# Performance work log

Hardware: AMD Instinct MI355X
Metric: run time of the kernel (lower is better)

The kernel has to match this reference:

```python
import jax, jax.numpy as jnp
import numpy as np

B, D, H = 131072, 256, 256
E, K, R = 4, 2, 5


def setup_inputs() -> dict:
    key = jax.random.key(0)
    ks = jax.random.split(key, 10)
    z = jax.random.normal(ks[0], (B, D), dtype=jnp.float32)
    centroids = jax.random.normal(ks[1], (R, E, D), dtype=jnp.float32) * 0.5
    tau_raw = jnp.full((R,), np.log(np.e - 1.0), dtype=jnp.float32)  # softplus(tau_raw)=1.0
    # Expert FFN params (Linear init ~ U(-1/sqrt(fan_in), 1/sqrt(fan_in)))
    s1 = 1.0 / np.sqrt(D)
    s2 = 1.0 / np.sqrt(H)
    W1 = jax.random.uniform(ks[2], (E, D, H), dtype=jnp.float32, minval=-s1, maxval=s1)
    b1 = jax.random.uniform(ks[3], (E, H), dtype=jnp.float32, minval=-s1, maxval=s1)
    W2 = jax.random.uniform(ks[4], (E, H, D), dtype=jnp.float32, minval=-s2, maxval=s2)
    b2 = jax.random.uniform(ks[5], (E, D), dtype=jnp.float32, minval=-s2, maxval=s2)
    ln_gamma = jnp.ones((D,), dtype=jnp.float32)
    ln_beta = jnp.zeros((D,), dtype=jnp.float32)
    return {"z": z, "router_idx": 2, "centroids": centroids, "tau_raw": tau_raw,
            "W1": W1, "b1": b1, "W2": W2, "b2": b2,
            "ln_gamma": ln_gamma, "ln_beta": ln_beta}


def reference(z, router_idx, centroids, tau_raw, W1, b1, W2, b2, ln_gamma, ln_beta):
    num_experts = W1.shape[0]
    top_k = K
    c = centroids[router_idx]                       # (E, D)
    tau = jax.nn.softplus(tau_raw[router_idx]) + 1e-6
    # Laplace-kernel gating: exp(-||z - c||_2 / tau)
    dist = jnp.sqrt(jnp.sum((z[:, None, :] - c[None, :, :]) ** 2, axis=-1))  # (B, E)
    scores = jnp.exp(-dist / tau)
    top_scores, top_idx = jax.lax.top_k(scores, top_k)          # (B, K)
    weights = jax.nn.softmax(top_scores, axis=-1)               # (B, K)
    # Dense all-expert FFN (E is tiny), then gather the top-k outputs.
    h = jax.nn.gelu(jnp.einsum('bd,edh->beh', z, W1) + b1[None], approximate=False)
    expert_out = jnp.einsum('beh,ehd->bed', h, W2) + b2[None]   # (B, E, D)
    sel = jnp.take_along_axis(expert_out, top_idx[:, :, None], axis=1)  # (B, K, D)
    moe_out = jnp.sum(weights[:, :, None] * sel, axis=1)        # (B, D)
    # Residual + LayerNorm (eps = 1e-5 as in torch)
    x = z + moe_out
    mu = jnp.mean(x, axis=-1, keepdims=True)
    var = jnp.mean((x - mu) ** 2, axis=-1, keepdims=True)
    y = ln_gamma * (x - mu) / jnp.sqrt(var + 1e-5) + ln_beta
    # Expert utilization (training-mode output)
    counts = jnp.sum(jax.nn.one_hot(top_idx, num_experts, dtype=jnp.float32), axis=(0, 1))
    expert_weights = counts / (z.shape[0] * top_k)
    return y, expert_weights
```

## Files before the change

### kernel.cpp

```cpp
#include <hip/hip_runtime.h>
#include <hip/hip_bf16.h>
#include <math.h>

#define Bz 131072
#define Dd 256

typedef __attribute__((ext_vector_type(8))) short short8;
typedef __attribute__((ext_vector_type(4))) float f32x4;
typedef __attribute__((ext_vector_type(4))) unsigned short u16x4;
typedef __attribute__((ext_vector_type(8))) unsigned short u16x8;

__device__ __forceinline__ unsigned short f2bf(float f) {
    union { __hip_bfloat16 h; unsigned short u; } v;
    v.h = __float2bfloat16(f);
    return v.u;
}
__device__ __forceinline__ float bf2f(unsigned short h) {
    union { unsigned int u; float f; } v; v.u = ((unsigned int)h) << 16;
    return v.f;
}
__device__ __forceinline__ float gelu_f(float x) {
    float u = 0.7978845608028654f * x * (1.0f + 0.044715f * x * x);
    float ex = __builtin_amdgcn_exp2f(u * 2.8853900817779268f);
    float th = 1.0f - 2.0f * __builtin_amdgcn_rcpf(1.0f + ex);
    return 0.5f * x * (1.0f + th);
}

#define MFMA16(a, b, c) __builtin_amdgcn_mfma_f32_16x16x32_bf16(a, b, c, 0, 0, 0)

__global__ __launch_bounds__(256) void prep_kernel(const float* __restrict__ W1,
                                                   const float* __restrict__ W2,
                                                   unsigned short* __restrict__ W1s,
                                                   unsigned short* __restrict__ W2s,
                                                   unsigned int* __restrict__ ctr) {
    __shared__ float tile[32][257];
    int bid = blockIdx.x;
    int tid = threadIdx.x;
    if (bid == 0 && tid < 16) ctr[tid] = 0u;
    int mat = bid >> 5, e = (bid >> 3) & 3, tn = bid & 7;
    const float* src = (mat ? W2 : W1) + e * 65536;
    unsigned short* dst = (mat ? W2s : W1s) + e * 65536 + tn * 8192;
#pragma unroll 4
    for (int kk = 0; kk < 32; ++kk)
        tile[kk][tid] = src[(tn * 32 + kk) * 256 + tid];
    __syncthreads();
#pragma unroll 4
    for (int oo = 0; oo < 32; ++oo) {
        int o = oo * 256 + tid;
        int u = o >> 11, c = (o >> 3) & 255, j = o & 7;
        dst[o] = f2bf(tile[u * 8 + j][c]);
    }
}

__global__ __launch_bounds__(256) void gate_kernel(const float* __restrict__ z,
                                                   const int* __restrict__ ridx_p,
                                                   const float* __restrict__ centroids,
                                                   const float* __restrict__ tau_raw,
                                                   float* __restrict__ wdense,
                                                   unsigned int* __restrict__ ctr) {
    __shared__ unsigned int scnt[4];
    __shared__ unsigned int shist[6];
    int tid = threadIdx.x;
    if (tid < 4) scnt[tid] = 0u;
    if (tid < 6) shist[tid] = 0u;
    __syncthreads();
    int lane = tid & 63;
    int gwave = (blockIdx.x * 256 + tid) >> 6;
    int ridx = ridx_p[0];
    double tau = log1p(exp((double)tau_raw[ridx])) + 1e-6;
    const float* cb = centroids + (size_t)ridx * (4 * Dd);
    float c[4][4];
#pragma unroll
    for (int e = 0; e < 4; ++e) {
        f32x4 cv = *(const f32x4*)(cb + e * 256 + lane * 4);
#pragma unroll
        for (int j = 0; j < 4; ++j) c[e][j] = cv[j];
    }
    for (int rr = 0; rr < 16; ++rr) {
        int row = gwave * 16 + rr;
        f32x4 zv = *(const f32x4*)(z + (size_t)row * 256 + lane * 4);
        double d2[4] = {0.0, 0.0, 0.0, 0.0};
#pragma unroll
        for (int e = 0; e < 4; ++e)
#pragma unroll
            for (int j = 0; j < 4; ++j) {
                double df = (double)zv[j] - (double)c[e][j];
                d2[e] += df * df;
            }
#pragma unroll
        for (int m = 32; m >= 1; m >>= 1)
#pragma unroll
            for (int e = 0; e < 4; ++e) d2[e] += __shfl_xor(d2[e], m, 64);
        if (lane == 0) {
            int e1 = 0;
#pragma unroll
            for (int e = 1; e < 4; ++e) if (d2[e] < d2[e1]) e1 = e;
            int e2 = (e1 == 0) ? 1 : 0;
#pragma unroll
            for (int e = 0; e < 4; ++e)
                if (e != e1 && e != e2 && d2[e] < d2[e2]) e2 = e;
            double s1 = exp(-sqrt(d2[e1]) / tau);
            double s2 = exp(-sqrt(d2[e2]) / tau);
            double w1 = 1.0 / (1.0 + exp(s2 - s1));
            f32x4 wv;
#pragma unroll
            for (int j = 0; j < 4; ++j)
                wv[j] = (j == e1) ? (float)w1 : ((j == e2) ? (float)(1.0 - w1) : 0.0f);
            *(f32x4*)(wdense + (size_t)row * 4) = wv;
            int el = e1 < e2 ? e1 : e2;
            int eh = e1 < e2 ? e2 : e1;
            int pidx = (el == 0) ? (eh - 1) : ((el == 1) ? (eh + 1) : 5);
            atomicAdd(&shist[pidx], 1u);
            atomicAdd(&scnt[e1], 1u);
            atomicAdd(&scnt[e2], 1u);
        }
    }
    __syncthreads();
    if (tid < 4) atomicAdd(&ctr[tid], scnt[tid]);
    if (tid < 6) atomicAdd(&ctr[4 + tid], shist[tid]);
}

__global__ void offsets_kernel(unsigned int* __restrict__ ctr, int* __restrict__ perm) {
    __shared__ int sb[7], sh[6];
    int t = threadIdx.x;
    if (t == 0) {
        int base = 0;
        for (int p = 0; p < 6; ++p) {
            sb[p] = base;
            sh[p] = (int)ctr[4 + p];
            base += (sh[p] + 47) / 48 * 48;
        }
        sb[6] = base;
        for (int p = 0; p < 7; ++p) ctr[16 + p] = (unsigned int)sb[p];
    }
    if (t < 6) ctr[10 + t] = 0u;
    __syncthreads();
    for (int p = 0; p < 6; ++p)
        for (int s = sb[p] + sh[p] + t; s < sb[p + 1]; s += 64)
            perm[s] = -1;
}

__global__ __launch_bounds__(256) void scatter_kernel(const float* __restrict__ wdense,
                                                      unsigned int* __restrict__ ctr,
                                                      int* __restrict__ perm) {
    __shared__ unsigned int lcnt[6];
    __shared__ unsigned int lbase[6];
    int tid = threadIdx.x;
    if (tid < 6) lcnt[tid] = 0u;
    __syncthreads();
    int r = blockIdx.x * 256 + tid;
    f32x4 w = *(const f32x4*)(wdense + (size_t)r * 4);
    int el = -1, eh = -1;
#pragma unroll
    for (int e = 0; e < 4; ++e)
        if (w[e] != 0.0f) { if (el < 0) el = e; else eh = e; }
    int pidx = (el == 0) ? (eh - 1) : ((el == 1) ? (eh + 1) : 5);
    unsigned int local = atomicAdd(&lcnt[pidx], 1u);
    __syncthreads();
    if (tid < 6) lbase[tid] = atomicAdd(&ctr[10 + tid], lcnt[tid]);
    __syncthreads();
    perm[ctr[16 + pidx] + lbase[pidx] + local] = r;
}

__global__ __launch_bounds__(512, 4) void ffn_kernel(const float* __restrict__ z,
    const unsigned short* __restrict__ W1s, const unsigned short* __restrict__ W2s,
    const float* __restrict__ b1, const float* __restrict__ b2,
    const float* __restrict__ wdense, const float* __restrict__ ln_g,
    const float* __restrict__ ln_b, const unsigned int* __restrict__ ctr,
    const int* __restrict__ perm, float* __restrict__ y) {
    __shared__ char zls[24576];
    __shared__ char h1s[24576];
    __shared__ int ridx_s[48];
    __shared__ float wa_s[48], wb_s[48];
    __shared__ float ps[8][56], pq[8][56];

    int slot0 = blockIdx.x * 48;
    int total = (int)ctr[22];
    if (slot0 >= total) return;
    int p = 0;
#pragma unroll
    for (int q = 1; q < 6; ++q) if (slot0 >= (int)ctr[16 + q]) p = q;
    int ea = (p < 3) ? 0 : ((p < 5) ? 1 : 2);
    int eb = (p < 3) ? (p + 1) : ((p < 5) ? (p - 1) : 3);

    int tid = threadIdx.x;
    int lane = tid & 63, wv = tid >> 6;
    int ln15 = lane & 15, lhi = lane >> 4;
    int l7 = ln15 & 7;
    int nbase = wv * 32;

    const unsigned short* g1a = W1s + (ea << 16);
    const unsigned short* g2a = W2s + (ea << 16);
    const unsigned short* g1b = W1s + (eb << 16);
    const unsigned short* g2b = W2s + (eb << 16);

    if (tid < 48) {
        int g = perm[slot0 + tid];
        ridx_s[tid] = g;
        int g2 = (g < 0) ? 0 : g;
        wa_s[tid] = wdense[(size_t)g2 * 4 + ea];
        wb_s[tid] = wdense[(size_t)g2 * 4 + eb];
    }
    __syncthreads();

#pragma unroll
    for (int it = 0; it < 3; ++it) {
        int idx = it * 512 + tid;
        int r = idx >> 5, sl = idx & 31;
        int g = ridx_s[r]; if (g < 0) g = 0;
        f32x4 v0 = *(const f32x4*)(z + (size_t)g * 256 + sl * 8);
        f32x4 v1 = *(const f32x4*)(z + (size_t)g * 256 + sl * 8 + 4);
        u16x8 hv;
        hv[0] = f2bf(v0[0]); hv[1] = f2bf(v0[1]); hv[2] = f2bf(v0[2]); hv[3] = f2bf(v0[3]);
        hv[4] = f2bf(v1[0]); hv[5] = f2bf(v1[1]); hv[6] = f2bf(v1[2]); hv[7] = f2bf(v1[3]);
        *(u16x8*)(&zls[r * 512 + ((sl ^ (r & 7)) << 4)]) = hv;
    }
    __syncthreads();

    u16x4 zrv[2][3];
#pragma unroll
    for (int fm = 0; fm < 2; ++fm) {
        int d0 = nbase + fm * 16 + lhi * 4;
        int dsl = d0 >> 3, db = (d0 & 7) * 2;
#pragma unroll
        for (int fn = 0; fn < 3; ++fn) {
            int row = fn * 16 + ln15;
            zrv[fm][fn] = *(const u16x4*)(&zls[row * 512 + ((dsl ^ (row & 7)) << 4) + db]);
        }
    }

    int wfo = lhi * 2048 + (nbase + ln15) * 8;

    auto gemm_phase = [&](const unsigned short* g0, const char* bsrc, f32x4 (&dst)[2][3]) {
        short8 a0c = *(const short8*)(g0 + wfo);
        short8 a1c = *(const short8*)(g0 + wfo + 128);
        short8 a0m = *(const short8*)(g0 + 8192 + wfo);
        short8 a1m = *(const short8*)(g0 + 8192 + wfo + 128);
#pragma unroll
        for (int tn = 0; tn < 8; ++tn) {
            short8 a0n, a1n;
            if (tn < 6) {
                a0n = *(const short8*)(g0 + (tn + 2) * 8192 + wfo);
                a1n = *(const short8*)(g0 + (tn + 2) * 8192 + wfo + 128);
            }
            int sl = ((tn * 4 + lhi) ^ l7) << 4;
            {
                short8 bv0 = *(const short8*)(bsrc + (ln15) * 512 + sl);
                short8 bv1 = *(const short8*)(bsrc + (16 + ln15) * 512 + sl);
                __builtin_amdgcn_s_setprio(1);
                dst[0][0] = MFMA16(a0c, bv0, dst[0][0]);
                dst[1][0] = MFMA16(a1c, bv0, dst[1][0]);
                dst[0][1] = MFMA16(a0c, bv1, dst[0][1]);
                dst[1][1] = MFMA16(a1c, bv1, dst[1][1]);
                __builtin_amdgcn_s_setprio(0);
            }
            {
                short8 bv2 = *(const short8*)(bsrc + (32 + ln15) * 512 + sl);
                __builtin_amdgcn_s_setprio(1);
                dst[0][2] = MFMA16(a0c, bv2, dst[0][2]);
                dst[1][2] = MFMA16(a1c, bv2, dst[1][2]);
                __builtin_amdgcn_s_setprio(0);
            }
            a0c = a0m; a1c = a1m;
            if (tn < 6) { a0m = a0n; a1m = a1n; }
        }
    };

    {
        f32x4 acc1[2][3];
        auto epi = [&](const float* b1e, const float* wsel, char* dst) {
#pragma unroll
            for (int fm = 0; fm < 2; ++fm) {
                int h0 = nbase + fm * 16 + lhi * 4;
                int hsl = h0 >> 3, hb = (h0 & 7) * 2;
                f32x4 b1f = *(const f32x4*)(b1e + h0);
#pragma unroll
                for (int fn = 0; fn < 3; ++fn) {
                    int row = fn * 16 + ln15;
                    float w = wsel[row];
                    u16x4 hv;
#pragma unroll
                    for (int i = 0; i < 4; ++i)
                        hv[i] = f2bf(gelu_f(acc1[fm][fn][i] + b1f[i]) * w);
                    *(u16x4*)(&dst[row * 512 + ((hsl ^ (row & 7)) << 4) + hb]) = hv;
                }
            }
        };
#pragma unroll
        for (int i = 0; i < 2; ++i)
#pragma unroll
            for (int j = 0; j < 3; ++j) acc1[i][j] = (f32x4)0.0f;
        gemm_phase(g1a, zls, acc1);
        epi(b1 + (ea << 8), wa_s, h1s);
#pragma unroll
        for (int i = 0; i < 2; ++i)
#pragma unroll
            for (int j = 0; j < 3; ++j) acc1[i][j] = (f32x4)0.0f;
        gemm_phase(g1b, zls, acc1);
        __syncthreads();
        epi(b1 + (eb << 8), wb_s, zls);
        __syncthreads();
    }

    f32x4 acc[2][3];
#pragma unroll
    for (int i = 0; i < 2; ++i)
#pragma unroll
        for (int j = 0; j < 3; ++j) acc[i][j] = (f32x4)0.0f;
    gemm_phase(g2a, h1s, acc);
    gemm_phase(g2b, zls, acc);

    float sA[3] = {0.0f, 0.0f, 0.0f};
    float sB[3] = {0.0f, 0.0f, 0.0f};
#pragma unroll
    for (int fm = 0; fm < 2; ++fm) {
        int d0 = nbase + fm * 16 + lhi * 4;
        f32x4 ba = *(const f32x4*)(b2 + (ea << 8) + d0);
        f32x4 bb = *(const f32x4*)(b2 + (eb << 8) + d0);
#pragma unroll
        for (int fn = 0; fn < 3; ++fn) {
            int row = fn * 16 + ln15;
            float wa = wa_s[row], wb = wb_s[row];
#pragma unroll
            for (int i = 0; i < 4; ++i) {
                float x = acc[fm][fn][i] + wa * ba[i] + wb * bb[i] + bf2f(zrv[fm][fn][i]);
                acc[fm][fn][i] = x;
                sA[fn] += x;
                sB[fn] += x * x;
            }
        }
    }
#pragma unroll
    for (int fn = 0; fn < 3; ++fn) {
        sA[fn] += __shfl_xor(sA[fn], 16, 64);
        sA[fn] += __shfl_xor(sA[fn], 32, 64);
        sB[fn] += __shfl_xor(sB[fn], 16, 64);
        sB[fn] += __shfl_xor(sB[fn], 32, 64);
    }
    if (lhi < 3) {
        float v1 = (lhi == 0) ? sA[0] : (lhi == 1) ? sA[1] : sA[2];
        float v2 = (lhi == 0) ? sB[0] : (lhi == 1) ? sB[1] : sB[2];
        int row = lhi * 16 + ln15;
        ps[wv][row] = v1;
        pq[wv][row] = v2;
    }
    __syncthreads();

    float mu[3], rs[3];
#pragma unroll
    for (int fn = 0; fn < 3; ++fn) {
        int row = fn * 16 + ln15;
        float s = 0.0f, q = 0.0f;
#pragma unroll
        for (int j = 0; j < 8; ++j) { s += ps[j][row]; q += pq[j][row]; }
        float m = s * (1.0f / 256.0f);
        float var = q * (1.0f / 256.0f) - m * m;
        mu[fn] = m;
        rs[fn] = rsqrtf(var + 1e-5f);
    }
#pragma unroll
    for (int fm = 0; fm < 2; ++fm) {
        int d0 = nbase + fm * 16 + lhi * 4;
        f32x4 gm = *(const f32x4*)(ln_g + d0);
        f32x4 bt = *(const f32x4*)(ln_b + d0);
#pragma unroll
        for (int fn = 0; fn < 3; ++fn) {
            int row = fn * 16 + ln15;
            int g = ridx_s[row];
            if (g >= 0) {
                f32x4 yv;
#pragma unroll
                for (int i = 0; i < 4; ++i)
                    yv[i] = gm[i] * ((acc[fm][fn][i] - mu[fn]) * rs[fn]) + bt[i];
                *(f32x4*)(y + (size_t)g * 256 + d0) = yv;
            }
        }
    }
}

__global__ void final_kernel(const unsigned int* __restrict__ ctr, float* __restrict__ out) {
    int t = threadIdx.x;
    if (t < 4) out[(size_t)Bz * Dd + t] = (float)ctr[t] * (1.0f / 262144.0f);
}

extern "C" void kernel_launch(void* const* d_in, const int* in_sizes, int n_in,
                              void* d_out, int out_size, void* d_ws, size_t ws_size,
                              hipStream_t stream) {
    const float* z         = (const float*)d_in[0];
    const int*   ridx      = (const int*)d_in[1];
    const float* centroids = (const float*)d_in[2];
    const float* tau_raw   = (const float*)d_in[3];
    const float* W1        = (const float*)d_in[4];
    const float* b1        = (const float*)d_in[5];
    const float* W2        = (const float*)d_in[6];
    const float* b2        = (const float*)d_in[7];
    const float* lng       = (const float*)d_in[8];
    const float* lnb       = (const float*)d_in[9];
    float* out = (float*)d_out;

    unsigned short* W1s    = (unsigned short*)d_ws;
    unsigned short* W2s    = (unsigned short*)((char*)d_ws + 524288);
    float*          wdense = (float*)((char*)d_ws + 1048576);
    int*            perm   = (int*)((char*)d_ws + 3145728);
    unsigned int*   ctr    = (unsigned int*)((char*)d_ws + 3672064);

    hipLaunchKernelGGL(prep_kernel, dim3(64), dim3(256), 0, stream, W1, W2, W1s, W2s, ctr);
    hipLaunchKernelGGL(gate_kernel, dim3(2048), dim3(256), 0, stream, z, ridx, centroids, tau_raw, wdense, ctr);
    hipLaunchKernelGGL(offsets_kernel, dim3(1), dim3(64), 0, stream, ctr, perm);
    hipLaunchKernelGGL(scatter_kernel, dim3(512), dim3(256), 0, stream, wdense, ctr, perm);
    hipLaunchKernelGGL(ffn_kernel, dim3(2744), dim3(512), 0, stream, z, W1s, W2s, b1, b2, wdense, lng, lnb, ctr, perm, out);
    hipLaunchKernelGGL(final_kernel, dim3(1), dim3(64), 0, stream, ctr, out);
}
```

Before: 232.2 us.

## Compute gate distances via norm expansion with 16-lane row groups; widen prep grid

Measured after the change: 199.7 us. -14.0%, faster.

```diff
diff --git a/kernel.cpp b/kernel.cpp
--- a/kernel.cpp
+++ b/kernel.cpp
@@ -37,16 +37,16 @@
     int bid = blockIdx.x;
     int tid = threadIdx.x;
     if (bid == 0 && tid < 16) ctr[tid] = 0u;
-    int mat = bid >> 5, e = (bid >> 3) & 3, tn = bid & 7;
+    int mat = bid >> 7, e = (bid >> 5) & 3, tn = (bid >> 2) & 7, qq = bid & 3;
     const float* src = (mat ? W2 : W1) + e * 65536;
     unsigned short* dst = (mat ? W2s : W1s) + e * 65536 + tn * 8192;
 #pragma unroll 4
     for (int kk = 0; kk < 32; ++kk)
         tile[kk][tid] = src[(tn * 32 + kk) * 256 + tid];
     __syncthreads();
-#pragma unroll 4
-    for (int oo = 0; oo < 32; ++oo) {
-        int o = oo * 256 + tid;
+#pragma unroll
+    for (int oo = 0; oo < 8; ++oo) {
+        int o = (qq * 8 + oo) * 256 + tid;
         int u = o >> 11, c = (o >> 3) & 255, j = o & 7;
         dst[o] = f2bf(tile[u * 8 + j][c]);
     }
@@ -65,33 +65,63 @@
     if (tid < 6) shist[tid] = 0u;
     __syncthreads();
     int lane = tid & 63;
+    int l16 = lane & 15, grp = lane >> 4;
     int gwave = (blockIdx.x * 256 + tid) >> 6;
+    int rbase = gwave * 16;
     int ridx = ridx_p[0];
     double tau = log1p(exp((double)tau_raw[ridx])) + 1e-6;
     const float* cb = centroids + (size_t)ridx * (4 * Dd);
-    float c[4][4];
+
+    float c[4][16];
+#pragma unroll
+    for (int e = 0; e < 4; ++e)
+#pragma unroll
+        for (int q = 0; q < 4; ++q) {
+            f32x4 cv = *(const f32x4*)(cb + e * 256 + l16 * 16 + q * 4);
+#pragma unroll
+            for (int j = 0; j < 4; ++j) c[e][q * 4 + j] = cv[j];
+        }
+    double cn[4];
 #pragma unroll
     for (int e = 0; e < 4; ++e) {
-        f32x4 cv = *(const f32x4*)(cb + e * 256 + lane * 4);
-#pragma unroll
-        for (int j = 0; j < 4; ++j) c[e][j] = cv[j];
-    }
-    for (int rr = 0; rr < 16; ++rr) {
-        int row = gwave * 16 + rr;
-        f32x4 zv = *(const f32x4*)(z + (size_t)row * 256 + lane * 4);
-        double d2[4] = {0.0, 0.0, 0.0, 0.0};
-#pragma unroll
-        for (int e = 0; e < 4; ++e)
+        double s = 0.0;
+#pragma unroll
+        for (int j = 0; j < 16; ++j) {
+            double cc = (double)c[e][j];
+            s += cc * cc;
+        }
+#pragma unroll
+        for (int m = 1; m < 16; m <<= 1) s += __shfl_xor(s, m, 64);
+        cn[e] = s;
+    }
+
+    for (int it = 0; it < 4; ++it) {
+        int row = rbase + it * 4 + grp;
+        const float* zr = z + (size_t)row * 256 + l16 * 16;
+        double dot[4] = {0.0, 0.0, 0.0, 0.0};
+        double zn = 0.0;
+#pragma unroll
+        for (int q = 0; q < 4; ++q) {
+            f32x4 zv = *(const f32x4*)(zr + q * 4);
 #pragma unroll
             for (int j = 0; j < 4; ++j) {
-                double df = (double)zv[j] - (double)c[e][j];
-                d2[e] += df * df;
-            }
-#pragma unroll
-        for (int m = 32; m >= 1; m >>= 1)
-#pragma unroll
-            for (int e = 0; e < 4; ++e) d2[e] += __shfl_xor(d2[e], m, 64);
-        if (lane == 0) {
+                double zz = (double)zv[j];
+                zn += zz * zz;
+#pragma unroll
+                for (int e = 0; e < 4; ++e)
+                    dot[e] += zz * (double)c[e][q * 4 + j];
+            }
+        }
+#pragma unroll
+        for (int m = 1; m < 16; m <<= 1) {
+            zn += __shfl_xor(zn, m, 64);
+#pragma unroll
+            for (int e = 0; e < 4; ++e) dot[e] += __shfl_xor(dot[e], m, 64);
+        }
+        if (l16 == 0) {
+            double d2[4];
+#pragma unroll
+            for (int e = 0; e < 4; ++e) d2[e] = cn[e] - 2.0 * dot[e] + zn;
             int e1 = 0;
 #pragma unroll
             for (int e = 1; e < 4; ++e) if (d2[e] < d2[e1]) e1 = e;
@@ -404,7 +434,7 @@
     int*            perm   = (int*)((char*)d_ws + 3145728);
     unsigned int*   ctr    = (unsigned int*)((char*)d_ws + 3672064);
 
-    hipLaunchKernelGGL(prep_kernel, dim3(64), dim3(256), 0, stream, W1, W2, W1s, W2s, ctr);
+    hipLaunchKernelGGL(prep_kernel, dim3(256), dim3(256), 0, stream, W1, W2, W1s, W2s, ctr);
     hipLaunchKernelGGL(gate_kernel, dim3(2048), dim3(256), 0, stream, z, ridx, centroids, tau_raw, wdense, ctr);
     hipLaunchKernelGGL(offsets_kernel, dim3(1), dim3(64), 0, stream, ctr, perm);
     hipLaunchKernelGGL(scatter_kernel, dim3(512), dim3(256), 0, stream, wdense, ctr, perm);
```
